# Performance work log

Hardware: AMD Instinct MI355X
Metric: run time of the kernel (lower is better)

The kernel has to match this reference:

```python
import jax, jax.numpy as jnp
import numpy as np

N, E = 50000, 800000
IN_C, HID, OUT_C, HEADS = 256, 32, 16, 8
NEG_SLOPE = 0.2


def gat_conv(x, edge_index, W, att_src, att_dst, bias, heads, out_c, concat):
    """PyG-style GATConv (inference, dropout off, add_self_loops=True).

    x: [N, F_in], edge_index: [2, E] with row0=src(j), row1=dst(i).
    W: [F_in, heads*out_c], att_src/att_dst: [heads, out_c], bias: [heads*out_c] or [out_c].
    """
    n = x.shape[0]
    loops = jnp.arange(n, dtype=edge_index.dtype)
    src = jnp.concatenate([edge_index[0], loops])
    dst = jnp.concatenate([edge_index[1], loops])

    xl = (x @ W).reshape(n, heads, out_c)              # [N, H, C]
    a_src = jnp.einsum('nhc,hc->nh', xl, att_src)      # [N, H]
    a_dst = jnp.einsum('nhc,hc->nh', xl, att_dst)

    e = a_src[src] + a_dst[dst]                        # [E', H]
    e = jnp.where(e >= 0, e, NEG_SLOPE * e)            # leaky_relu
    e_max = jax.ops.segment_max(e, dst, num_segments=n)
    e_exp = jnp.exp(e - e_max[dst])
    denom = jax.ops.segment_sum(e_exp, dst, num_segments=n)
    alpha = e_exp / (denom[dst] + 1e-16)               # segment softmax over in-edges of dst

    msg = alpha[:, :, None] * xl[src]                  # [E', H, C]
    out = jax.ops.segment_sum(msg, dst, num_segments=n)  # [N, H, C]
    if concat:
        out = out.reshape(n, heads * out_c)
    else:
        out = out.mean(axis=1)
    return out + bias


def setup_inputs() -> dict:
    key = jax.random.key(0)
    ks = jax.random.split(key, 10)
    s_in = 1.0 / np.sqrt(IN_C)
    s_h = 1.0 / np.sqrt(HEADS * HID)
    x = jax.random.normal(ks[0], (N, IN_C), dtype=jnp.float32)
    edge_index = jax.random.randint(ks[1], (2, E), 0, N, dtype=jnp.int64)
    return {
        'x': x,
        'edge_index': edge_index,
        'W1': jax.random.normal(ks[2], (IN_C, HEADS * HID), dtype=jnp.float32) * s_in,
        'att_src1': jax.random.normal(ks[3], (HEADS, HID), dtype=jnp.float32) * s_h,
        'att_dst1': jax.random.normal(ks[4], (HEADS, HID), dtype=jnp.float32) * s_h,
        'b1': jnp.zeros((HEADS * HID,), dtype=jnp.float32),
        'W2': jax.random.normal(ks[5], (HEADS * HID, OUT_C), dtype=jnp.float32) * s_h,
        'att_src2': jax.random.normal(ks[6], (1, OUT_C), dtype=jnp.float32) * 0.1,
        'att_dst2': jax.random.normal(ks[7], (1, OUT_C), dtype=jnp.float32) * 0.1,
        'b2': jnp.zeros((OUT_C,), dtype=jnp.float32),
    }


def reference(x, edge_index, W1, att_src1, att_dst1, b1, W2, att_src2, att_dst2, b2):
    h = gat_conv(x, edge_index, W1, att_src1, att_dst1, b1, HEADS, HID, concat=True)
    h = jax.nn.relu(h)
    # F.dropout(training=False) is identity at inference
    out = gat_conv(h, edge_index, W2, att_src2, att_dst2, b2, 1, OUT_C, concat=False)
    return jax.nn.log_softmax(out, axis=1)
```

## Files before the change

### kernel.cpp

```cpp
#include <hip/hip_runtime.h>

#define IN_C 256
#define H1 8
#define C1 32
#define F1 256
#define OC 16
#define NEG 0.2f

typedef short short8 __attribute__((ext_vector_type(8)));
typedef unsigned short ushort8 __attribute__((ext_vector_type(8)));
typedef float floatx4 __attribute__((ext_vector_type(4)));

__device__ __forceinline__ unsigned short f2bf(float f) {
    unsigned u = __builtin_bit_cast(unsigned, f);
    u = (u + 0x7fffu + ((u >> 16) & 1u)) >> 16;
    return (unsigned short)u;
}
__device__ __forceinline__ float bf2f(unsigned short h) {
    unsigned u = ((unsigned)h) << 16;
    return __builtin_bit_cast(float, u);
}

__global__ __launch_bounds__(256) void k_cvt_x(const float* __restrict__ x,
                                               unsigned short* __restrict__ xb, int n4)
{
    int idx = blockIdx.x * 256 + threadIdx.x;
    if (idx >= n4) return;
    float4 v = ((const float4*)x)[idx];
    ushort4 o;
    o.x = f2bf(v.x); o.y = f2bf(v.y); o.z = f2bf(v.z); o.w = f2bf(v.w);
    ((ushort4*)xb)[idx] = o;
}

__global__ __launch_bounds__(256) void k_w1t(const float* __restrict__ W1,
                                             unsigned short* __restrict__ w1t)
{
    int idx = blockIdx.x * 256 + threadIdx.x;
    int n = idx >> 8, k = idx & 255;
    w1t[n * 256 + k] = f2bf(W1[k * 256 + n]);
}

__global__ __launch_bounds__(256) void k_gemm1(const unsigned short* __restrict__ A,
                                               const unsigned short* __restrict__ Bt,
                                               unsigned short* __restrict__ Cb, int M)
{
    __shared__ short As[128][40];
    __shared__ short Bs[128][40];
    const int tid  = threadIdx.x;
    const int lane = tid & 63;
    const int w    = tid >> 6;
    const int bm   = blockIdx.x * 128;
    const int bn   = blockIdx.y * 128;
    const int wm   = (w >> 1) * 64;
    const int wn   = (w & 1) * 64;
    const int srow = tid >> 1;
    const int soff = (tid & 1) * 16;
    floatx4 acc[4][4] = {};
    for (int k0 = 0; k0 < 256; k0 += 32) {
        __syncthreads();
        {
            int gr = bm + srow;
            ushort8 v0 = {0,0,0,0,0,0,0,0}, v1 = {0,0,0,0,0,0,0,0};
            if (gr < M) {
                const ushort8* p = (const ushort8*)(A + (size_t)gr * 256 + k0 + soff);
                v0 = p[0]; v1 = p[1];
            }
            *(ushort8*)&As[srow][soff]     = v0;
            *(ushort8*)&As[srow][soff + 8] = v1;
        }
        {
            const ushort8* p = (const ushort8*)(Bt + (size_t)(bn + srow) * 256 + k0 + soff);
            *(ushort8*)&Bs[srow][soff]     = p[0];
            *(ushort8*)&Bs[srow][soff + 8] = p[1];
        }
        __syncthreads();
        short8 af[4], bf[4];
        const int q8 = (lane >> 4) * 8;
        const int l15 = lane & 15;
#pragma unroll
        for (int i = 0; i < 4; ++i) af[i] = *(const short8*)&As[wm + i * 16 + l15][q8];
#pragma unroll
        for (int j = 0; j < 4; ++j) bf[j] = *(const short8*)&Bs[wn + j * 16 + l15][q8];
#pragma unroll
        for (int i = 0; i < 4; ++i)
#pragma unroll
            for (int j = 0; j < 4; ++j)
                acc[i][j] = __builtin_amdgcn_mfma_f32_16x16x32_bf16(af[i], bf[j], acc[i][j], 0, 0, 0);
    }
    const int l15 = lane & 15;
    const int rq  = (lane >> 4) * 4;
#pragma unroll
    for (int i = 0; i < 4; ++i) {
#pragma unroll
        for (int reg = 0; reg < 4; ++reg) {
            int gr = bm + wm + i * 16 + rq + reg;
            if (gr < M) {
#pragma unroll
                for (int j = 0; j < 4; ++j)
                    Cb[(size_t)gr * 256 + bn + wn + j * 16 + l15] = f2bf(acc[i][j][reg]);
            }
        }
    }
}

__global__ __launch_bounds__(256) void k_att1(const unsigned short* __restrict__ xl,
                                              const float* __restrict__ att_s,
                                              const float* __restrict__ att_d,
                                              float* __restrict__ asrc,
                                              float* __restrict__ adst, int N)
{
    int idx = blockIdx.x * 256 + threadIdx.x;
    if (idx >= N * H1) return;
    int i = idx >> 3, h = idx & 7;
    const ushort4* xr = (const ushort4*)(xl + (size_t)i * F1 + h * C1);
    const float* s = att_s + h * C1;
    const float* d = att_d + h * C1;
    float s1 = 0.f, s2 = 0.f;
#pragma unroll
    for (int c4 = 0; c4 < 8; ++c4) {
        ushort4 v = xr[c4];
        float f0 = bf2f(v.x), f1 = bf2f(v.y), f2 = bf2f(v.z), f3 = bf2f(v.w);
        int c = c4 * 4;
        s1 += f0 * s[c] + f1 * s[c+1] + f2 * s[c+2] + f3 * s[c+3];
        s2 += f0 * d[c] + f1 * d[c+1] + f2 * d[c+2] + f3 * d[c+3];
    }
    asrc[idx] = s1; adst[idx] = s2;
}

__global__ __launch_bounds__(256) void k_zero(int* __restrict__ p, int n)
{
    int i = blockIdx.x * 256 + threadIdx.x;
    if (i < n) p[i] = 0;
}

__global__ __launch_bounds__(256) void k_hist(const int* __restrict__ ei,
                                              int* __restrict__ cnt, int E)
{
    int e = blockIdx.x * 256 + threadIdx.x;
    if (e < E) atomicAdd(&cnt[ei[E + e]], 1);
}

__global__ __launch_bounds__(1024) void k_scan(const int* __restrict__ cnt,
                                               int* __restrict__ rp, int N)
{
    __shared__ int wsum[16];
    __shared__ int carry_s;
    int lane = threadIdx.x & 63, wid = threadIdx.x >> 6;
    if (threadIdx.x == 0) { carry_s = 0; rp[0] = 0; }
    __syncthreads();
    for (int base = 0; base < N; base += 4096) {
        int i0 = base + threadIdx.x * 4;
        int v[4];
#pragma unroll
        for (int k = 0; k < 4; ++k) { int i = i0 + k; v[k] = (i < N) ? cnt[i] : 0; }
        int s = v[0] + v[1] + v[2] + v[3];
        int incl = s;
#pragma unroll
        for (int off = 1; off < 64; off <<= 1) {
            int t = __shfl_up(incl, off, 64);
            if (lane >= off) incl += t;
        }
        if (lane == 63) wsum[wid] = incl;
        __syncthreads();
        int wpre = 0;
        for (int ww = 0; ww < wid; ++ww) wpre += wsum[ww];
        int carry = carry_s;
        int run = carry + wpre + incl - s;
#pragma unroll
        for (int k = 0; k < 4; ++k) {
            int i = i0 + k;
            run += v[k];
            if (i < N) rp[i + 1] = run;
        }
        __syncthreads();
        if (threadIdx.x == 1023) carry_s = carry + wpre + incl;
        __syncthreads();
    }
}

__global__ __launch_bounds__(256) void k_scatter(const int* __restrict__ ei,
                                                 const int* __restrict__ rp,
                                                 int* __restrict__ cur,
                                                 int* __restrict__ ssrc, int E)
{
    int e = blockIdx.x * 256 + threadIdx.x;
    if (e >= E) return;
    int s = ei[e];
    int d = ei[E + e];
    int pos = rp[d] + atomicAdd(&cur[d], 1);
    ssrc[pos] = s;
}

__global__ __launch_bounds__(256) void k_gather1(const int* __restrict__ rp,
                                                 const int* __restrict__ ssrc,
                                                 const unsigned short* __restrict__ xl,
                                                 const float* __restrict__ asrc,
                                                 const float* __restrict__ adst,
                                                 const float* __restrict__ bias,
                                                 unsigned short* __restrict__ hout, int N)
{
    int lane = threadIdx.x & 63;
    int node = blockIdx.x * 4 + (threadIdx.x >> 6);
    if (node >= N) return;
    int h  = lane >> 3;
    int cb = lane * 4;
    float ad = adst[(size_t)node * H1 + h];
    float e = asrc[(size_t)node * H1 + h] + ad;
    e = e >= 0.f ? e : NEG * e;
    float w = __expf(e);
    ushort4 xv = *(const ushort4*)(xl + (size_t)node * F1 + cb);
    float ax = w * bf2f(xv.x), ay = w * bf2f(xv.y), az = w * bf2f(xv.z), aw = w * bf2f(xv.w);
    float den = w;
    int jb = rp[node], je = rp[node + 1];
    int j = jb;
    for (; j + 4 <= je; j += 4) {
        int s0 = ssrc[j], s1 = ssrc[j+1], s2 = ssrc[j+2], s3 = ssrc[j+3];
        float e0 = asrc[(size_t)s0 * H1 + h] + ad;
        float e1 = asrc[(size_t)s1 * H1 + h] + ad;
        float e2 = asrc[(size_t)s2 * H1 + h] + ad;
        float e3 = asrc[(size_t)s3 * H1 + h] + ad;
        ushort4 r0 = *(const ushort4*)(xl + (size_t)s0 * F1 + cb);
        ushort4 r1 = *(const ushort4*)(xl + (size_t)s1 * F1 + cb);
        ushort4 r2 = *(const ushort4*)(xl + (size_t)s2 * F1 + cb);
        ushort4 r3 = *(const ushort4*)(xl + (size_t)s3 * F1 + cb);
        e0 = e0 >= 0.f ? e0 : NEG * e0;  float w0 = __expf(e0);
        e1 = e1 >= 0.f ? e1 : NEG * e1;  float w1 = __expf(e1);
        e2 = e2 >= 0.f ? e2 : NEG * e2;  float w2 = __expf(e2);
        e3 = e3 >= 0.f ? e3 : NEG * e3;  float w3 = __expf(e3);
        den += w0 + w1 + w2 + w3;
        ax += w0*bf2f(r0.x) + w1*bf2f(r1.x) + w2*bf2f(r2.x) + w3*bf2f(r3.x);
        ay += w0*bf2f(r0.y) + w1*bf2f(r1.y) + w2*bf2f(r2.y) + w3*bf2f(r3.y);
        az += w0*bf2f(r0.z) + w1*bf2f(r1.z) + w2*bf2f(r2.z) + w3*bf2f(r3.z);
        aw += w0*bf2f(r0.w) + w1*bf2f(r1.w) + w2*bf2f(r2.w) + w3*bf2f(r3.w);
    }
    for (; j < je; ++j) {
        int s = ssrc[j];
        float ev = asrc[(size_t)s * H1 + h] + ad;
        ev = ev >= 0.f ? ev : NEG * ev;
        float wv = __expf(ev);
        ushort4 sv = *(const ushort4*)(xl + (size_t)s * F1 + cb);
        ax += wv * bf2f(sv.x); ay += wv * bf2f(sv.y);
        az += wv * bf2f(sv.z); aw += wv * bf2f(sv.w);
        den += wv;
    }
    float inv = 1.f / (den + 1e-16f);
    float4 bv = *(const float4*)(bias + cb);
    ushort4 o;
    o.x = f2bf(fmaxf(ax * inv + bv.x, 0.f));
    o.y = f2bf(fmaxf(ay * inv + bv.y, 0.f));
    o.z = f2bf(fmaxf(az * inv + bv.z, 0.f));
    o.w = f2bf(fmaxf(aw * inv + bv.w, 0.f));
    *(ushort4*)(hout + (size_t)node * F1 + cb) = o;
}

__global__ __launch_bounds__(256) void k_gemm2(const unsigned short* __restrict__ Hm,
                                               const float* __restrict__ W2,
                                               const float* __restrict__ as2,
                                               const float* __restrict__ ad2,
                                               float* __restrict__ xl2,
                                               float* __restrict__ asrc,
                                               float* __restrict__ adst, int N)
{
    __shared__ float Ws[F1 * OC];
    __shared__ float Hs[16 * F1];
    int tid = threadIdx.x;
    int base = blockIdx.x * 16;
    for (int idx = tid; idx < F1 * OC; idx += 256) Ws[idx] = W2[idx];
    for (int idx = tid; idx < 16 * F1; idx += 256) {
        int r = idx >> 8, k = idx & 255;
        int gr = base + r;
        Hs[idx] = (gr < N) ? bf2f(Hm[(size_t)gr * F1 + k]) : 0.f;
    }
    __syncthreads();
    int r = tid >> 4, c = tid & 15;
    float acc = 0.f;
#pragma unroll 8
    for (int k = 0; k < F1; ++k) acc += Hs[r * F1 + k] * Ws[k * OC + c];
    int gr = base + r;
    float s1 = acc * as2[c], s2 = acc * ad2[c];
#pragma unroll
    for (int o = 1; o < 16; o <<= 1) { s1 += __shfl_xor(s1, o, 16); s2 += __shfl_xor(s2, o, 16); }
    if (gr < N) {
        xl2[(size_t)gr * OC + c] = acc;
        if (c == 0) { asrc[gr] = s1; adst[gr] = s2; }
    }
}

__global__ __launch_bounds__(256) void k_gather2(const int* __restrict__ rp,
                                                 const int* __restrict__ ssrc,
                                                 const float* __restrict__ xl2,
                                                 const float* __restrict__ asrc,
                                                 const float* __restrict__ adst,
                                                 const float* __restrict__ bias,
                                                 float* __restrict__ out, int N)
{
    int sub  = threadIdx.x & 15;
    int node = blockIdx.x * 16 + (threadIdx.x >> 4);
    if (node >= N) return;
    float ad = adst[node];
    float e = asrc[node] + ad;
    e = e >= 0.f ? e : NEG * e;
    float w = __expf(e);
    float acc = w * xl2[(size_t)node * OC + sub];
    float den = w;
    int jb = rp[node], je = rp[node + 1];
    int j = jb;
    for (; j + 4 <= je; j += 4) {
        int s0 = ssrc[j], s1i = ssrc[j+1], s2i = ssrc[j+2], s3i = ssrc[j+3];
        float e0 = asrc[s0] + ad, e1 = asrc[s1i] + ad, e2 = asrc[s2i] + ad, e3 = asrc[s3i] + ad;
        float v0 = xl2[(size_t)s0 * OC + sub];
        float v1 = xl2[(size_t)s1i * OC + sub];
        float v2 = xl2[(size_t)s2i * OC + sub];
        float v3 = xl2[(size_t)s3i * OC + sub];
        e0 = e0 >= 0.f ? e0 : NEG * e0;  float w0 = __expf(e0);
        e1 = e1 >= 0.f ? e1 : NEG * e1;  float w1 = __expf(e1);
        e2 = e2 >= 0.f ? e2 : NEG * e2;  float w2 = __expf(e2);
        e3 = e3 >= 0.f ? e3 : NEG * e3;  float w3 = __expf(e3);
        den += w0 + w1 + w2 + w3;
        acc += w0 * v0 + w1 * v1 + w2 * v2 + w3 * v3;
    }
    for (; j < je; ++j) {
        int s = ssrc[j];
        float ev = asrc[s] + ad;
        ev = ev >= 0.f ? ev : NEG * ev;
        float wv = __expf(ev);
        acc += wv * xl2[(size_t)s * OC + sub];
        den += wv;
    }
    float v = acc / (den + 1e-16f) + bias[sub];
    float m = v;
#pragma unroll
    for (int o = 1; o < 16; o <<= 1) m = fmaxf(m, __shfl_xor(m, o, 16));
    float ex = __expf(v - m);
    float ss = ex;
#pragma unroll
    for (int o = 1; o < 16; o <<= 1) ss += __shfl_xor(ss, o, 16);
    out[(size_t)node * OC + sub] = v - m - logf(ss);
}

extern "C" void kernel_launch(void* const* d_in, const int* in_sizes, int n_in,
                              void* d_out, int out_size, void* d_ws, size_t ws_size,
                              hipStream_t stream)
{
    const float* x   = (const float*)d_in[0];
    const int*   ei  = (const int*)d_in[1];
    const float* W1  = (const float*)d_in[2];
    const float* as1 = (const float*)d_in[3];
    const float* ad1 = (const float*)d_in[4];
    const float* b1  = (const float*)d_in[5];
    const float* W2  = (const float*)d_in[6];
    const float* as2 = (const float*)d_in[7];
    const float* ad2 = (const float*)d_in[8];
    const float* b2  = (const float*)d_in[9];
    float* out = (float*)d_out;

    const int N = in_sizes[0] / IN_C;
    const int E = in_sizes[1] / 2;

    char* base = (char*)d_ws;
    unsigned short* xb   = (unsigned short*)base;
    unsigned short* xl1b = xb + (size_t)N * F1;
    unsigned short* hb   = xl1b + (size_t)N * F1;
    unsigned short* w1t  = hb + (size_t)N * F1;
    float* asrc1 = (float*)(w1t + 256 * 256);
    float* adst1 = asrc1 + (size_t)N * H1;
    float* xl2   = adst1 + (size_t)N * H1;
    float* asrc2 = xl2 + (size_t)N * OC;
    float* adst2 = asrc2 + N;
    int*   rp    = (int*)(adst2 + N);
    int*   cnt   = rp + (N + 1);
    int*   cur   = cnt + N;
    int*   ssrc  = cur + N;

    k_zero<<<(2 * N + 255) / 256, 256, 0, stream>>>(cnt, 2 * N);
    k_hist<<<(E + 255) / 256, 256, 0, stream>>>(ei, cnt, E);
    k_scan<<<1, 1024, 0, stream>>>(cnt, rp, N);
    k_scatter<<<(E + 255) / 256, 256, 0, stream>>>(ei, rp, cur, ssrc, E);

    k_cvt_x<<<(N * 64 + 255) / 256, 256, 0, stream>>>(x, xb, N * 64);
    k_w1t<<<256, 256, 0, stream>>>(W1, w1t);

    k_gemm1<<<dim3((N + 127) / 128, 2), 256, 0, stream>>>(xb, w1t, xl1b, N);
    k_att1<<<(N * H1 + 255) / 256, 256, 0, stream>>>(xl1b, as1, ad1, asrc1, adst1, N);
    k_gather1<<<(N + 3) / 4, 256, 0, stream>>>(rp, ssrc, xl1b, asrc1, adst1, b1, hb, N);

    k_gemm2<<<(N + 15) / 16, 256, 0, stream>>>(hb, W2, as2, ad2, xl2, asrc2, adst2, N);
    k_gather2<<<(N + 15) / 16, 256, 0, stream>>>(rp, ssrc, xl2, asrc2, adst2, b2, out, N);
}
```

Before: 385.2 us.

## Parallelize CSR scan, use MFMA for second GEMM, store layer-2 features as bf16

```diff
diff --git a/kernel.cpp b/kernel.cpp
--- a/kernel.cpp
+++ b/kernel.cpp
@@ -32,12 +32,20 @@
     ((ushort4*)xb)[idx] = o;
 }
 
-__global__ __launch_bounds__(256) void k_w1t(const float* __restrict__ W1,
-                                             unsigned short* __restrict__ w1t)
+__global__ __launch_bounds__(256) void k_wcvt(const float* __restrict__ W1,
+                                              const float* __restrict__ W2,
+                                              unsigned short* __restrict__ w1t,
+                                              unsigned short* __restrict__ w2t)
 {
     int idx = blockIdx.x * 256 + threadIdx.x;
-    int n = idx >> 8, k = idx & 255;
-    w1t[n * 256 + k] = f2bf(W1[k * 256 + n]);
+    if (idx < 65536) {
+        int n = idx >> 8, k = idx & 255;
+        w1t[n * 256 + k] = f2bf(W1[k * 256 + n]);
+    } else if (idx < 65536 + 4096) {
+        int r = idx - 65536;
+        int n = r >> 8, k = r & 255;
+        w2t[n * 256 + k] = f2bf(W2[k * 16 + n]);
+    }
 }
 
 __global__ __launch_bounds__(256) void k_gemm1(const unsigned short* __restrict__ A,
@@ -127,12 +135,6 @@
     asrc[idx] = s1; adst[idx] = s2;
 }
 
-__global__ __launch_bounds__(256) void k_zero(int* __restrict__ p, int n)
-{
-    int i = blockIdx.x * 256 + threadIdx.x;
-    if (i < n) p[i] = 0;
-}
-
 __global__ __launch_bounds__(256) void k_hist(const int* __restrict__ ei,
                                               int* __restrict__ cnt, int E)
 {
@@ -140,46 +142,67 @@
     if (e < E) atomicAdd(&cnt[ei[E + e]], 1);
 }
 
-__global__ __launch_bounds__(1024) void k_scan(const int* __restrict__ cnt,
-                                               int* __restrict__ rp, int N)
-{
-    __shared__ int wsum[16];
-    __shared__ int carry_s;
-    int lane = threadIdx.x & 63, wid = threadIdx.x >> 6;
-    if (threadIdx.x == 0) { carry_s = 0; rp[0] = 0; }
+__global__ __launch_bounds__(256) void k_scan_a(const int* __restrict__ cnt,
+                                                int* __restrict__ rp,
+                                                int* __restrict__ bsum, int N)
+{
+    __shared__ int ws4[4];
+    int t = threadIdx.x, lane = t & 63, wid = t >> 6;
+    int i = blockIdx.x * 256 + t;
+    int v = (i < N) ? cnt[i] : 0;
+    int incl = v;
+#pragma unroll
+    for (int off = 1; off < 64; off <<= 1) {
+        int tv = __shfl_up(incl, off, 64);
+        if (lane >= off) incl += tv;
+    }
+    if (lane == 63) ws4[wid] = incl;
     __syncthreads();
-    for (int base = 0; base < N; base += 4096) {
-        int i0 = base + threadIdx.x * 4;
-        int v[4];
-#pragma unroll
-        for (int k = 0; k < 4; ++k) { int i = i0 + k; v[k] = (i < N) ? cnt[i] : 0; }
-        int s = v[0] + v[1] + v[2] + v[3];
-        int incl = s;
-#pragma unroll
-        for (int off = 1; off < 64; off <<= 1) {
-            int t = __shfl_up(incl, off, 64);
-            if (lane >= off) incl += t;
-        }
-        if (lane == 63) wsum[wid] = incl;
-        __syncthreads();
-        int wpre = 0;
-        for (int ww = 0; ww < wid; ++ww) wpre += wsum[ww];
-        int carry = carry_s;
-        int run = carry + wpre + incl - s;
-#pragma unroll
-        for (int k = 0; k < 4; ++k) {
-            int i = i0 + k;
-            run += v[k];
-            if (i < N) rp[i + 1] = run;
-        }
-        __syncthreads();
-        if (threadIdx.x == 1023) carry_s = carry + wpre + incl;
-        __syncthreads();
-    }
+    int add = 0;
+    for (int w = 0; w < wid; ++w) add += ws4[w];
+    incl += add;
+    if (i < N) rp[i + 1] = incl;
+    if (t == 255) bsum[blockIdx.x] = incl;
+}
+
+__global__ __launch_bounds__(256) void k_scan_b(const int* __restrict__ bsum,
+                                                int* __restrict__ boff, int NB)
+{
+    __shared__ int ws4[4];
+    int t = threadIdx.x, lane = t & 63, wid = t >> 6;
+    int i0 = t * 4;
+    int v[4];
+#pragma unroll
+    for (int k = 0; k < 4; ++k) { int i = i0 + k; v[k] = (i < NB) ? bsum[i] : 0; }
+    int s = v[0] + v[1] + v[2] + v[3];
+    int incl = s;
+#pragma unroll
+    for (int off = 1; off < 64; off <<= 1) {
+        int tv = __shfl_up(incl, off, 64);
+        if (lane >= off) incl += tv;
+    }
+    if (lane == 63) ws4[wid] = incl;
+    __syncthreads();
+    int wpre = 0;
+    for (int w = 0; w < wid; ++w) wpre += ws4[w];
+    int run = wpre + incl - s;
+#pragma unroll
+    for (int k = 0; k < 4; ++k) {
+        int i = i0 + k;
+        if (i < NB) boff[i] = run;
+        run += v[k];
+    }
+}
+
+__global__ __launch_bounds__(256) void k_scan_c(int* __restrict__ rp,
+                                                const int* __restrict__ boff, int N)
+{
+    int i = blockIdx.x * 256 + threadIdx.x;
+    if (i < N) rp[i + 1] += boff[blockIdx.x];
+    if (i == 0) rp[0] = 0;
 }
 
 __global__ __launch_bounds__(256) void k_scatter(const int* __restrict__ ei,
-                                                 const int* __restrict__ rp,
                                                  int* __restrict__ cur,
                                                  int* __restrict__ ssrc, int E)
 {
@@ -187,7 +210,7 @@
     if (e >= E) return;
     int s = ei[e];
     int d = ei[E + e];
-    int pos = rp[d] + atomicAdd(&cur[d], 1);
+    int pos = atomicAdd(&cur[d], 1);
     ssrc[pos] = s;
 }
 
@@ -254,41 +277,49 @@
 }
 
 __global__ __launch_bounds__(256) void k_gemm2(const unsigned short* __restrict__ Hm,
-                                               const float* __restrict__ W2,
+                                               const unsigned short* __restrict__ W2t,
                                                const float* __restrict__ as2,
                                                const float* __restrict__ ad2,
-                                               float* __restrict__ xl2,
+                                               unsigned short* __restrict__ xl2b,
                                                float* __restrict__ asrc,
                                                float* __restrict__ adst, int N)
 {
-    __shared__ float Ws[F1 * OC];
-    __shared__ float Hs[16 * F1];
-    int tid = threadIdx.x;
-    int base = blockIdx.x * 16;
-    for (int idx = tid; idx < F1 * OC; idx += 256) Ws[idx] = W2[idx];
-    for (int idx = tid; idx < 16 * F1; idx += 256) {
-        int r = idx >> 8, k = idx & 255;
-        int gr = base + r;
-        Hs[idx] = (gr < N) ? bf2f(Hm[(size_t)gr * F1 + k]) : 0.f;
-    }
-    __syncthreads();
-    int r = tid >> 4, c = tid & 15;
-    float acc = 0.f;
-#pragma unroll 8
-    for (int k = 0; k < F1; ++k) acc += Hs[r * F1 + k] * Ws[k * OC + c];
-    int gr = base + r;
-    float s1 = acc * as2[c], s2 = acc * ad2[c];
-#pragma unroll
-    for (int o = 1; o < 16; o <<= 1) { s1 += __shfl_xor(s1, o, 16); s2 += __shfl_xor(s2, o, 16); }
-    if (gr < N) {
-        xl2[(size_t)gr * OC + c] = acc;
-        if (c == 0) { asrc[gr] = s1; adst[gr] = s2; }
+    const int lane = threadIdx.x & 63;
+    const int wid  = threadIdx.x >> 6;
+    const int rowbase = blockIdx.x * 64 + wid * 16;
+    const int col = lane & 15;
+    const int q8  = (lane >> 4) * 8;
+    const int m   = rowbase + col;
+    const bool mv = m < N;
+    const unsigned short* arow = Hm + (size_t)m * 256 + q8;
+    const unsigned short* brow = W2t + (size_t)col * 256 + q8;
+    floatx4 acc = {0.f, 0.f, 0.f, 0.f};
+#pragma unroll
+    for (int t = 0; t < 8; ++t) {
+        short8 af = {0,0,0,0,0,0,0,0};
+        if (mv) af = *(const short8*)(arow + t * 32);
+        short8 bf = *(const short8*)(brow + t * 32);
+        acc = __builtin_amdgcn_mfma_f32_16x16x32_bf16(af, bf, acc, 0, 0, 0);
+    }
+    float s_as = as2[col], s_ad = ad2[col];
+    const int rq = (lane >> 4) * 4;
+#pragma unroll
+    for (int reg = 0; reg < 4; ++reg) {
+        int row = rowbase + rq + reg;
+        float v = acc[reg];
+        float s1 = v * s_as, s2 = v * s_ad;
+#pragma unroll
+        for (int o = 1; o < 16; o <<= 1) { s1 += __shfl_xor(s1, o, 16); s2 += __shfl_xor(s2, o, 16); }
+        if (row < N) {
+            xl2b[(size_t)row * OC + col] = f2bf(v);
+            if (col == 0) { asrc[row] = s1; adst[row] = s2; }
+        }
     }
 }
 
 __global__ __launch_bounds__(256) void k_gather2(const int* __restrict__ rp,
                                                  const int* __restrict__ ssrc,
-                                                 const float* __restrict__ xl2,
+                                                 const unsigned short* __restrict__ xl2b,
                                                  const float* __restrict__ asrc,
                                                  const float* __restrict__ adst,
                                                  const float* __restrict__ bias,
@@ -301,17 +332,17 @@
     float e = asrc[node] + ad;
     e = e >= 0.f ? e : NEG * e;
     float w = __expf(e);
-    float acc = w * xl2[(size_t)node * OC + sub];
+    float acc = w * bf2f(xl2b[(size_t)node * OC + sub]);
     float den = w;
     int jb = rp[node], je = rp[node + 1];
     int j = jb;
     for (; j + 4 <= je; j += 4) {
         int s0 = ssrc[j], s1i = ssrc[j+1], s2i = ssrc[j+2], s3i = ssrc[j+3];
         float e0 = asrc[s0] + ad, e1 = asrc[s1i] + ad, e2 = asrc[s2i] + ad, e3 = asrc[s3i] + ad;
-        float v0 = xl2[(size_t)s0 * OC + sub];
-        float v1 = xl2[(size_t)s1i * OC + sub];
-        float v2 = xl2[(size_t)s2i * OC + sub];
-        float v3 = xl2[(size_t)s3i * OC + sub];
+        float v0 = bf2f(xl2b[(size_t)s0 * OC + sub]);
+        float v1 = bf2f(xl2b[(size_t)s1i * OC + sub]);
+        float v2 = bf2f(xl2b[(size_t)s2i * OC + sub]);
+        float v3 = bf2f(xl2b[(size_t)s3i * OC + sub]);
         e0 = e0 >= 0.f ? e0 : NEG * e0;  float w0 = __expf(e0);
         e1 = e1 >= 0.f ? e1 : NEG * e1;  float w1 = __expf(e1);
         e2 = e2 >= 0.f ? e2 : NEG * e2;  float w2 = __expf(e2);
@@ -324,7 +355,7 @@
         float ev = asrc[s] + ad;
         ev = ev >= 0.f ? ev : NEG * ev;
         float wv = __expf(ev);
-        acc += wv * xl2[(size_t)s * OC + sub];
+        acc += wv * bf2f(xl2b[(size_t)s * OC + sub]);
         den += wv;
     }
     float v = acc / (den + 1e-16f) + bias[sub];
@@ -356,34 +387,41 @@
 
     const int N = in_sizes[0] / IN_C;
     const int E = in_sizes[1] / 2;
+    const int NB = (N + 255) / 256;
 
     char* base = (char*)d_ws;
     unsigned short* xb   = (unsigned short*)base;
     unsigned short* xl1b = xb + (size_t)N * F1;
     unsigned short* hb   = xl1b + (size_t)N * F1;
     unsigned short* w1t  = hb + (size_t)N * F1;
-    float* asrc1 = (float*)(w1t + 256 * 256);
+    unsigned short* w2t  = w1t + 256 * 256;
+    unsigned short* xl2b = w2t + 16 * 256;
+    float* asrc1 = (float*)(xl2b + (size_t)N * OC);
     float* adst1 = asrc1 + (size_t)N * H1;
-    float* xl2   = adst1 + (size_t)N * H1;
-    float* asrc2 = xl2 + (size_t)N * OC;
+    float* asrc2 = adst1 + (size_t)N * H1;
     float* adst2 = asrc2 + N;
     int*   rp    = (int*)(adst2 + N);
     int*   cnt   = rp + (N + 1);
     int*   cur   = cnt + N;
-    int*   ssrc  = cur + N;
-
-    k_zero<<<(2 * N + 255) / 256, 256, 0, stream>>>(cnt, 2 * N);
+    int*   bsum  = cur + N;
+    int*   boff  = bsum + 1024;
+    int*   ssrc  = boff + 1024;
+
+    hipMemsetAsync(cnt, 0, (size_t)N * sizeof(int), stream);
     k_hist<<<(E + 255) / 256, 256, 0, stream>>>(ei, cnt, E);
-    k_scan<<<1, 1024, 0, stream>>>(cnt, rp, N);
-    k_scatter<<<(E + 255) / 256, 256, 0, stream>>>(ei, rp, cur, ssrc, E);
+    k_scan_a<<<NB, 256, 0, stream>>>(cnt, rp, bsum, N);
+    k_scan_b<<<1, 256, 0, stream>>>(bsum, boff, NB);
+    k_scan_c<<<NB, 256, 0, stream>>>(rp, boff, N);
+    hipMemcpyAsync(cur, rp, (size_t)N * sizeof(int), hipMemcpyDeviceToDevice, stream);
+    k_scatter<<<(E + 255) / 256, 256, 0, stream>>>(ei, cur, ssrc, E);
 
     k_cvt_x<<<(N * 64 + 255) / 256, 256, 0, stream>>>(x, xb, N * 64);
-    k_w1t<<<256, 256, 0, stream>>>(W1, w1t);
+    k_wcvt<<<(65536 + 4096) / 256, 256, 0, stream>>>(W1, W2, w1t, w2t);
 
     k_gemm1<<<dim3((N + 127) / 128, 2), 256, 0, stream>>>(xb, w1t, xl1b, N);
     k_att1<<<(N * H1 + 255) / 256, 256, 0, stream>>>(xl1b, as1, ad1, asrc1, adst1, N);
     k_gather1<<<(N + 3) / 4, 256, 0, stream>>>(rp, ssrc, xl1b, asrc1, adst1, b1, hb, N);
 
-    k_gemm2<<<(N + 15) / 16, 256, 0, stream>>>(hb, W2, as2, ad2, xl2, asrc2, adst2, N);
-    k_gather2<<<(N + 15) / 16, 256, 0, stream>>>(rp, ssrc, xl2, asrc2, adst2, b2, out, N);
-}
+    k_gemm2<<<(N + 63) / 64, 256, 0, stream>>>(hb, w2t, as2, ad2, xl2b, asrc2, adst2, N);
+    k_gather2<<<(N + 15) / 16, 256, 0, stream>>>(rp, ssrc, xl2b, asrc2, adst2, b2, out, N);
+}
```

Result: faster. 338.5 us (-12.1%).
